# Optimization experiments

Measured on AMD Instinct MI355X. Metric: run time of the kernel, lower is better.

Reference implementation:

```python
import jax, jax.numpy as jnp
import numpy as np


def setup_inputs() -> dict:
    key = jax.random.key(0)
    k1, k2, k3, k4 = jax.random.split(key, 4)
    B, H, S, D = 2, 16, 2048, 64
    q = jax.random.normal(k1, (B, H, S, D), dtype=jnp.float32)
    k = jax.random.normal(k2, (B, H, S, D), dtype=jnp.float32)
    v = jax.random.normal(k3, (B, H, S, D), dtype=jnp.float32)
    mask = jax.random.randint(k4, (1, 1, S, S), 0, 2, dtype=jnp.int32)
    return {"q": q, "k": k, "v": v, "mask": mask}


def reference(q, k, v, mask):
    # scores: [B,H,S,S] -- intentionally materialized as in the original
    d = k.shape[-1]
    scale = 1.0 / jnp.sqrt(jnp.asarray(d, dtype=q.dtype))
    x = jnp.einsum("bhqd,bhkd->bhqk", q, k) * scale
    x = x + mask.astype(x.dtype) * jnp.asarray(-10000.0, dtype=x.dtype)
    p = jax.nn.softmax(x, axis=-1)  # dropout is identity in eval mode
    return jnp.einsum("bhqk,bhkd->bhqd", p, v)
```

## Files before the change

kernel.cpp:

```cpp
#include <hip/hip_runtime.h>


#define S_LEN 2048
#define D_DIM 64
#define N_KT 32
#define NBH 32
#define TILE_SEGS 20
#define TILE_SHORTS_P (TILE_SEGS * 512)
#define K_SHORTS 4608
#define SEG_U32 256

typedef __attribute__((ext_vector_type(8))) short bf16x8;
typedef __attribute__((ext_vector_type(16))) float f32x16;
typedef __attribute__((ext_vector_type(2))) __fp16 fp16x2;
typedef unsigned int u32;

#define C1 0.180336880111121f
#define CM (-14426.9504088896f)

static __device__ __forceinline__ unsigned short f2bf(float f) {
  union { float f; unsigned u; } x; x.f = f;
  return (unsigned short)((x.u + 0x8000u) >> 16);
}
static __device__ __forceinline__ unsigned packbf(float lo, float hi) {
  union { float f; unsigned u; } a, b; a.f = lo; b.f = hi;
  return ((a.u + 0x8000u) >> 16) | ((b.u + 0x8000u) & 0xffff0000u);
}
static __device__ __forceinline__ f32x16 zero16() {
  f32x16 z;
#pragma unroll
  for (int i = 0; i < 16; ++i) z[i] = 0.f;
  return z;
}
static __device__ __forceinline__ void dma16(const u32* g, u32* l) {
  __builtin_amdgcn_global_load_lds(
      (const __attribute__((address_space(1))) u32*)g,
      (__attribute__((address_space(3))) u32*)l, 16, 0, 0);
}
static __device__ __forceinline__ unsigned pkh(float lo, float hi) {
  union { fp16x2 h; unsigned u; } x;
  x.h = __builtin_amdgcn_cvt_pkrtz(lo, hi);
  return x.u;
}

__global__ __launch_bounds__(256) void prep_kv(
    const float* __restrict__ k, const float* __restrict__ v,
    unsigned short* __restrict__ kvws) {
  const int kt = blockIdx.x, bh = blockIdx.y;
  const int t = threadIdx.x;
  __shared__ unsigned short Vt[K_SHORTS];
  const size_t goff = (size_t)bh * (S_LEN * D_DIM) + (size_t)kt * 64 * D_DIM;
  const float4* kg = (const float4*)(k + goff);
  const float4* vg = (const float4*)(v + goff);
  unsigned short* kimg = kvws + (size_t)(bh * N_KT + kt) * TILE_SHORTS_P;
#pragma unroll
  for (int j = 0; j < 4; ++j) {
    const int i = t + j * 256;
    const int row = i >> 4, c4 = i & 15;
    const float4 x = kg[i];
    ushort4 w;
    w.x = f2bf(x.x); w.y = f2bf(x.y); w.z = f2bf(x.z); w.w = f2bf(x.w);
    *(ushort4*)&kimg[row * 72 + c4 * 4] = w;
    const float4 y = vg[i];
    const int swc = 8 * (((row >> 3) + c4) & 7) + (row & 7);
    const unsigned p01 = pkh(y.x, y.y);
    const unsigned p23 = pkh(y.z, y.w);
    Vt[(4 * c4 + 0) * 72 + swc] = (unsigned short)(p01 & 0xffff);
    Vt[(4 * c4 + 1) * 72 + swc] = (unsigned short)(p01 >> 16);
    Vt[(4 * c4 + 2) * 72 + swc] = (unsigned short)(p23 & 0xffff);
    Vt[(4 * c4 + 3) * 72 + swc] = (unsigned short)(p23 >> 16);
  }
  __syncthreads();
  uint4* vimg = (uint4*)(kimg + K_SHORTS);
  const uint4* lv = (const uint4*)Vt;
  for (int i = t; i < K_SHORTS / 8; i += 256) vimg[i] = lv[i];
}

__global__ __launch_bounds__(256) void prep_mask(
    const int* __restrict__ mask, u32* __restrict__ mw) {
  const int gt = blockIdx.x * 256 + threadIdx.x;
  const int q4 = gt & 3;
  const int kt = (gt >> 2) & 31;
  const int hl = (gt >> 7) & 1;
  const int row = gt >> 8;
  const int j0 = kt * 64 + 32 * (q4 >> 1) + 16 * (q4 & 1) + 4 * hl;
  const int* mr = mask + (size_t)row * S_LEN;
  const int4 a = *(const int4*)(mr + j0);
  const int4 b = *(const int4*)(mr + j0 + 8);
  uint4 w;
  w.x = (a.x == 0 ? 0x0000FFFFu : 0u) | (a.y == 0 ? 0xFFFF0000u : 0u);
  w.y = (a.z == 0 ? 0x0000FFFFu : 0u) | (a.w == 0 ? 0xFFFF0000u : 0u);
  w.z = (b.x == 0 ? 0x0000FFFFu : 0u) | (b.y == 0 ? 0xFFFF0000u : 0u);
  w.w = (b.z == 0 ? 0x0000FFFFu : 0u) | (b.w == 0 ? 0xFFFF0000u : 0u);
  *(uint4*)&mw[((size_t)(row * 2 + hl) * N_KT + kt) * 16 + q4 * 4] = w;
}

__global__ __launch_bounds__(256, 4) void attn_fwd(
    const float* __restrict__ q, const unsigned short* __restrict__ kvws,
    const u32* __restrict__ mw, float* __restrict__ out) {
  const int qt = blockIdx.x;
  const int bh = blockIdx.y;
  const size_t hoff = (size_t)bh * (S_LEN * D_DIM);

  __shared__ unsigned short sbuf[2][TILE_SHORTS_P];

  const int t = threadIdx.x;
  const int wave = t >> 6;
  const int lane = t & 63;
  const int col = lane & 31;
  const int hl = lane >> 5;
  const int sw = col >> 2;
  const int qh = wave >> 1;
  const int kh = wave & 1;
  const int qg = qt * 64 + qh * 32 + col;

  bf16x8 bQ[4];
  {
    const float* qrow = q + hoff + (size_t)qg * D_DIM;
#pragma unroll
    for (int ks = 0; ks < 4; ++ks) {
      const float4 x0 = *(const float4*)(qrow + ks * 16 + hl * 8);
      const float4 x1 = *(const float4*)(qrow + ks * 16 + hl * 8 + 4);
      union { bf16x8 v; unsigned d[4]; } u;
      u.d[0] = packbf(x0.x * C1, x0.y * C1);
      u.d[1] = packbf(x0.z * C1, x0.w * C1);
      u.d[2] = packbf(x1.x * C1, x1.y * C1);
      u.d[3] = packbf(x1.z * C1, x1.w * C1);
      bQ[ks] = u.v;
    }
  }

  f32x16 oT0 = zero16(), oT1 = zero16();
  float lacc0 = 0.f, lacc1 = 0.f;
  const uint4* mrow = (const uint4*)(mw + (size_t)(qg * 2 + hl) * N_KT * 16);
  const u32* img = (const u32*)(kvws + (size_t)bh * N_KT * TILE_SHORTS_P);
  const int seg0 = wave * 5;

#if __has_builtin(__builtin_amdgcn_fdot2)
  const fp16x2 ones2 = {(__fp16)1.0f, (__fp16)1.0f};
#endif

  uint4 mq0, mq1;
  {
    const uint4* mp = mrow + kh * 2;
    asm volatile("global_load_dwordx4 %0, %2, off\n\t"
                 "global_load_dwordx4 %1, %3, off"
                 : "=&v"(mq0), "=&v"(mq1)
                 : "v"(mp), "v"(mp + 1)
                 : "memory");
  }
#pragma unroll
  for (int s = 0; s < 5; ++s)
    dma16(img + (size_t)(seg0 + s) * SEG_U32 + lane * 4,
          (u32*)&sbuf[0][0] + (seg0 + s) * SEG_U32);
#pragma unroll
  for (int s = 0; s < 5; ++s)
    dma16(img + (size_t)(TILE_SEGS + seg0 + s) * SEG_U32 + lane * 4,
          (u32*)&sbuf[1][0] + (seg0 + s) * SEG_U32);

  for (int kt = 0; kt < N_KT; ++kt) {
    const int p = kt & 1;
    if (kt < N_KT - 1) {
      asm volatile("s_waitcnt vmcnt(5)" ::: "memory");
    } else {
      asm volatile("s_waitcnt vmcnt(0)" ::: "memory");
    }
    __builtin_amdgcn_s_barrier();
    __builtin_amdgcn_sched_barrier(0);

    const unsigned short* Ksb = &sbuf[p][0];
    const unsigned short* Vtb = &sbuf[p][K_SHORTS];
    const u32 mwv[8] = {mq0.x, mq0.y, mq0.z, mq0.w,
                        mq1.x, mq1.y, mq1.z, mq1.w};

    f32x16 sT = zero16();
#pragma unroll
    for (int ks = 0; ks < 4; ++ks) {
      const bf16x8 aK =
          *(const bf16x8*)&Ksb[(kh * 32 + col) * 72 + ks * 16 + hl * 8];
      sT = __builtin_amdgcn_mfma_f32_32x32x16_bf16(aK, bQ[ks], sT, 0, 0, 0);
    }

    unsigned pw[8];
#pragma unroll
    for (int g2 = 0; g2 < 4; ++g2) {
      const float e0 = __builtin_amdgcn_exp2f(sT[g2 * 4 + 0]);
      const float e1 = __builtin_amdgcn_exp2f(sT[g2 * 4 + 1]);
      const float e2 = __builtin_amdgcn_exp2f(sT[g2 * 4 + 2]);
      const float e3 = __builtin_amdgcn_exp2f(sT[g2 * 4 + 3]);
#if __has_builtin(__builtin_amdgcn_fdot2)
      const unsigned w0 = pkh(e0, e1) & mwv[g2 * 2 + 0];
      const unsigned w1 = pkh(e2, e3) & mwv[g2 * 2 + 1];
      pw[g2 * 2 + 0] = w0;
      pw[g2 * 2 + 1] = w1;
      union { unsigned u; fp16x2 h; } c0, c1;
      c0.u = w0; c1.u = w1;
      lacc0 = __builtin_amdgcn_fdot2(c0.h, ones2, lacc0, false);
      lacc1 = __builtin_amdgcn_fdot2(c1.h, ones2, lacc1, false);
#else
      const u32 mlo = mwv[g2 * 2 + 0], mhi = mwv[g2 * 2 + 1];
      const float e0m = (mlo & 0xFFFFu) ? e0 : 0.f;
      const float e1m = (mlo >> 16) ? e1 : 0.f;
      const float e2m = (mhi & 0xFFFFu) ? e2 : 0.f;
      const float e3m = (mhi >> 16) ? e3 : 0.f;
      pw[g2 * 2 + 0] = pkh(e0m, e1m);
      pw[g2 * 2 + 1] = pkh(e2m, e3m);
      lacc0 += e0m + e1m;
      lacc1 += e2m + e3m;
#endif
    }

#pragma unroll
    for (int ks2 = 0; ks2 < 2; ++ks2) {
      const unsigned d0 = pw[4 * ks2 + 0], d1 = pw[4 * ks2 + 1];
      const unsigned d2 = pw[4 * ks2 + 2], d3 = pw[4 * ks2 + 3];
      const unsigned s0 = hl ? d0 : d2;
      const unsigned s1 = hl ? d1 : d3;
      const unsigned r0 = (unsigned)__shfl_xor((int)s0, 32);
      const unsigned r1 = (unsigned)__shfl_xor((int)s1, 32);
      union { bf16x8 v; unsigned d[4]; } pf;
      pf.d[0] = hl ? r0 : d0;
      pf.d[1] = hl ? r1 : d1;
      pf.d[2] = hl ? d2 : r0;
      pf.d[3] = hl ? d3 : r1;
      const int cpr = 8 * (((4 * kh + 2 * ks2 + hl) + sw) & 7);
      const bf16x8 aV0 = *(const bf16x8*)&Vtb[col * 72 + cpr];
      const bf16x8 aV1 = *(const bf16x8*)&Vtb[(32 + col) * 72 + cpr];
      oT0 = __builtin_amdgcn_mfma_f32_32x32x16_f16(aV0, pf.v, oT0, 0, 0, 0);
      oT1 = __builtin_amdgcn_mfma_f32_32x32x16_f16(aV1, pf.v, oT1, 0, 0, 0);
    }

    if (kt < N_KT - 1) {
      asm volatile("s_waitcnt lgkmcnt(0)" ::: "memory");
      __builtin_amdgcn_s_barrier();
      __builtin_amdgcn_sched_barrier(0);
      {
        const uint4* mp = mrow + (kt + 1) * 4 + kh * 2;
        asm volatile("global_load_dwordx4 %0, %2, off\n\t"
                     "global_load_dwordx4 %1, %3, off"
                     : "=&v"(mq0), "=&v"(mq1)
                     : "v"(mp), "v"(mp + 1)
                     : "memory");
      }
      if (kt < N_KT - 2) {
        const u32* g = img + (size_t)(kt + 2) * (TILE_SEGS * SEG_U32);
#pragma unroll
        for (int s = 0; s < 5; ++s)
          dma16(g + (size_t)(seg0 + s) * SEG_U32 + lane * 4,
                (u32*)&sbuf[p][0] + (seg0 + s) * SEG_U32);
      }
    }
  }

  __syncthreads();
  {
    float* xb = (float*)&sbuf[0][0];
    float* lb = (float*)((char*)&sbuf[0][0] + 17408);
    const float lsum = lacc0 + lacc1;
    const float l2 = lsum + __shfl_xor(lsum, 32);
    float* xr = xb + (size_t)(qh * 32 + col) * 68;
    if (kh) {
#pragma unroll
      for (int rg = 0; rg < 4; ++rg) {
        float4 w0, w1;
        w0.x = oT0[rg * 4 + 0]; w0.y = oT0[rg * 4 + 1];
        w0.z = oT0[rg * 4 + 2]; w0.w = oT0[rg * 4 + 3];
        w1.x = oT1[rg * 4 + 0]; w1.y = oT1[rg * 4 + 1];
        w1.z = oT1[rg * 4 + 2]; w1.w = oT1[rg * 4 + 3];
        *(float4*)(xr + 8 * rg + 4 * hl) = w0;
        *(float4*)(xr + 32 + 8 * rg + 4 * hl) = w1;
      }
      if (!hl) lb[qh * 32 + col] = l2;
    }
    __syncthreads();
    if (!kh) {
      const float inv = 1.0f / (l2 + lb[qh * 32 + col]);
      float* orow = out + hoff + (size_t)qg * D_DIM;
#pragma unroll
      for (int rg = 0; rg < 4; ++rg) {
        const float4 a0 = *(const float4*)(xr + 8 * rg + 4 * hl);
        const float4 a1 = *(const float4*)(xr + 32 + 8 * rg + 4 * hl);
        float4 w0, w1;
        w0.x = (oT0[rg * 4 + 0] + a0.x) * inv;
        w0.y = (oT0[rg * 4 + 1] + a0.y) * inv;
        w0.z = (oT0[rg * 4 + 2] + a0.z) * inv;
        w0.w = (oT0[rg * 4 + 3] + a0.w) * inv;
        w1.x = (oT1[rg * 4 + 0] + a1.x) * inv;
        w1.y = (oT1[rg * 4 + 1] + a1.y) * inv;
        w1.z = (oT1[rg * 4 + 2] + a1.z) * inv;
        w1.w = (oT1[rg * 4 + 3] + a1.w) * inv;
        *(float4*)(orow + 8 * rg + 4 * hl) = w0;
        *(float4*)(orow + 32 + 8 * rg + 4 * hl) = w1;
      }
    }
  }
}

#define LDK 72
#define LDV 72
__global__ __launch_bounds__(256, 2) void attn_fwd_self(
    const float* __restrict__ q, const float* __restrict__ k,
    const float* __restrict__ v, const int* __restrict__ mask,
    float* __restrict__ out) {
  const int qt = blockIdx.x;
  const int bh = blockIdx.y;
  const size_t hoff = (size_t)bh * (S_LEN * D_DIM);
  __shared__ unsigned short Ks[64 * LDK];
  __shared__ unsigned short Vt[64 * LDV];
  const int t = threadIdx.x;
  const int wave = t >> 6;
  const int lane = t & 63;
  const int col = lane & 31;
  const int hl = lane >> 5;
  const int sw = col >> 2;
  const int qg = qt * 128 + wave * 32 + col;
  bf16x8 bQ[4];
  {
    const float* qrow = q + hoff + (size_t)qg * D_DIM;
#pragma unroll
    for (int ks = 0; ks < 4; ++ks) {
      const float4 x0 = *(const float4*)(qrow + ks * 16 + hl * 8);
      const float4 x1 = *(const float4*)(qrow + ks * 16 + hl * 8 + 4);
      union { bf16x8 v; unsigned d[4]; } u;
      u.d[0] = packbf(x0.x, x0.y);
      u.d[1] = packbf(x0.z, x0.w);
      u.d[2] = packbf(x1.x, x1.y);
      u.d[3] = packbf(x1.z, x1.w);
      bQ[ks] = u.v;
    }
  }
  float4 pk[4], pv[4];
  {
    const float4* kg = (const float4*)(k + hoff);
    const float4* vg = (const float4*)(v + hoff);
#pragma unroll
    for (int j = 0; j < 4; ++j) { pk[j] = kg[t + j * 256]; pv[j] = vg[t + j * 256]; }
  }
  f32x16 oT0 = zero16(), oT1 = zero16();
  float lacc = 0.f;
  const int* mrow = mask + (size_t)qg * S_LEN;
  for (int kt = 0; kt < N_KT; ++kt) {
    __syncthreads();
#pragma unroll
    for (int j = 0; j < 4; ++j) {
      const int i = t + j * 256;
      const int row = i >> 4, c4 = i & 15;
      ushort4 w;
      w.x = f2bf(pk[j].x); w.y = f2bf(pk[j].y);
      w.z = f2bf(pk[j].z); w.w = f2bf(pk[j].w);
      *(ushort4*)&Ks[row * LDK + c4 * 4] = w;
      const int swc = 8 * (((row >> 3) + c4) & 7) + (row & 7);
      Vt[(4 * c4 + 0) * LDV + swc] = f2bf(pv[j].x);
      Vt[(4 * c4 + 1) * LDV + swc] = f2bf(pv[j].y);
      Vt[(4 * c4 + 2) * LDV + swc] = f2bf(pv[j].z);
      Vt[(4 * c4 + 3) * LDV + swc] = f2bf(pv[j].w);
    }
    __syncthreads();
    if (kt + 1 < N_KT) {
      const float4* kg = (const float4*)(k + hoff + (size_t)(kt + 1) * 64 * D_DIM);
      const float4* vg = (const float4*)(v + hoff + (size_t)(kt + 1) * 64 * D_DIM);
#pragma unroll
      for (int j = 0; j < 4; ++j) { pk[j] = kg[t + j * 256]; pv[j] = vg[t + j * 256]; }
    }
    int4 mq[2][4];
#pragma unroll
    for (int kb = 0; kb < 2; ++kb)
#pragma unroll
      for (int g = 0; g < 4; ++g)
        mq[kb][g] = *(const int4*)(mrow + kt * 64 + kb * 32 + g * 8 + hl * 4);
    f32x16 sT0 = zero16(), sT1 = zero16();
#pragma unroll
    for (int ks = 0; ks < 4; ++ks) {
      const bf16x8 aK0 = *(const bf16x8*)&Ks[col * LDK + ks * 16 + hl * 8];
      const bf16x8 aK1 = *(const bf16x8*)&Ks[(32 + col) * LDK + ks * 16 + hl * 8];
      sT0 = __builtin_amdgcn_mfma_f32_32x32x16_bf16(aK0, bQ[ks], sT0, 0, 0, 0);
      sT1 = __builtin_amdgcn_mfma_f32_32x32x16_bf16(aK1, bQ[ks], sT1, 0, 0, 0);
    }
    unsigned pw[2][8];
#pragma unroll
    for (int kb = 0; kb < 2; ++kb) {
      const f32x16 sT = kb ? sT1 : sT0;
      float e[16];
#pragma unroll
      for (int g = 0; g < 4; ++g) {
        const int4 mv = mq[kb][g];
        const int* mvp = &mv.x;
#pragma unroll
        for (int r3 = 0; r3 < 4; ++r3) {
          const int reg = g * 4 + r3;
          const float bias = mvp[r3] ? CM : 0.0f;
          const float ev = __builtin_amdgcn_exp2f(fmaf(sT[reg], C1, bias));
          e[reg] = ev;
          lacc += ev;
        }
        pw[kb][g * 2 + 0] = packbf(e[g * 4 + 0], e[g * 4 + 1]);
        pw[kb][g * 2 + 1] = packbf(e[g * 4 + 2], e[g * 4 + 3]);
      }
    }
#pragma unroll
    for (int ks = 0; ks < 4; ++ks) {
      const int kb = ks >> 1, h = ks & 1;
      const unsigned d0 = pw[kb][4 * h + 0], d1 = pw[kb][4 * h + 1];
      const unsigned d2 = pw[kb][4 * h + 2], d3 = pw[kb][4 * h + 3];
      const unsigned s0 = hl ? d0 : d2;
      const unsigned s1 = hl ? d1 : d3;
      const unsigned r0 = (unsigned)__shfl_xor((int)s0, 32);
      const unsigned r1 = (unsigned)__shfl_xor((int)s1, 32);
      union { bf16x8 v; unsigned d[4]; } pf;
      pf.d[0] = hl ? r0 : d0;
      pf.d[1] = hl ? r1 : d1;
      pf.d[2] = hl ? d2 : r0;
      pf.d[3] = hl ? d3 : r1;
      const int cpr = 8 * (((2 * ks + hl) + sw) & 7);
      const bf16x8 aV0 = *(const bf16x8*)&Vt[col * LDV + cpr];
      const bf16x8 aV1 = *(const bf16x8*)&Vt[(32 + col) * LDV + cpr];
      oT0 = __builtin_amdgcn_mfma_f32_32x32x16_bf16(aV0, pf.v, oT0, 0, 0, 0);
      oT1 = __builtin_amdgcn_mfma_f32_32x32x16_bf16(aV1, pf.v, oT1, 0, 0, 0);
    }
  }
  const float ltot = lacc + __shfl_xor(lacc, 32);
  const float inv = 1.0f / ltot;
  float* orow = out + hoff + (size_t)qg * D_DIM;
#pragma unroll
  for (int rg = 0; rg < 4; ++rg) {
    float4 w0, w1;
    w0.x = oT0[rg * 4 + 0] * inv; w0.y = oT0[rg * 4 + 1] * inv;
    w0.z = oT0[rg * 4 + 2] * inv; w0.w = oT0[rg * 4 + 3] * inv;
    w1.x = oT1[rg * 4 + 0] * inv; w1.y = oT1[rg * 4 + 1] * inv;
    w1.z = oT1[rg * 4 + 2] * inv; w1.w = oT1[rg * 4 + 3] * inv;
    *(float4*)(orow + 8 * rg + 4 * hl) = w0;
    *(float4*)(orow + 32 + 8 * rg + 4 * hl) = w1;
  }
}

extern "C" void kernel_launch(void* const* d_in, const int* in_sizes, int n_in,
                              void* d_out, int out_size, void* d_ws, size_t ws_size,
                              hipStream_t stream) {
  const float* q = (const float*)d_in[0];
  const float* k = (const float*)d_in[1];
  const float* v = (const float*)d_in[2];
  const int* mask = (const int*)d_in[3];
  float* out = (float*)d_out;

  const size_t kv_shorts = (size_t)NBH * N_KT * TILE_SHORTS_P;
  const size_t mw_words = (size_t)S_LEN * 2 * N_KT * 16;
  const size_t need = kv_shorts * sizeof(unsigned short) + mw_words * 4;

  if (ws_size >= need) {
    unsigned short* kvws = (unsigned short*)d_ws;
    u32* mwp = (u32*)(kvws + kv_shorts);
    prep_kv<<<dim3(N_KT, NBH), dim3(256), 0, stream>>>(k, v, kvws);
    prep_mask<<<dim3((S_LEN * 2 * N_KT * 4) / 256), dim3(256), 0, stream>>>(mask, mwp);
    attn_fwd<<<dim3(S_LEN / 64, NBH), dim3(256), 0, stream>>>(q, kvws, mwp, out);
  } else {
    attn_fwd_self<<<dim3(S_LEN / 128, NBH), dim3(256), 0, stream>>>(q, k, v, mask, out);
  }
}
```

Baseline: 167.3 us.

## Fuse KV and mask prep kernels and store K/V tiles in MFMA fragment order

The two preprocessing kernels are merged into one launch, with the block index deciding whether a block converts K/V or packs the mask. The K/V workspace image changes from padded 72-stride rows with swizzled V to a dense fragment-ordered layout, so each lane's MFMA operand is a contiguous 16-byte chunk. Tiles shrink from 20 to 16 segments, which cuts DMA traffic and LDS footprint per tile and removes the swizzle arithmetic in the main loop. The cost is more shuffling work in the prep kernel, including a scalar gather when transposing V.

```diff
diff --git a/kernel.cpp b/kernel.cpp
--- a/kernel.cpp
+++ b/kernel.cpp
@@ -5,9 +5,8 @@
 #define D_DIM 64
 #define N_KT 32
 #define NBH 32
-#define TILE_SEGS 20
-#define TILE_SHORTS_P (TILE_SEGS * 512)
-#define K_SHORTS 4608
+#define TILE_SEGS 16
+#define TILE_SHORTS 8192
 #define SEG_U32 256
 
 typedef __attribute__((ext_vector_type(8))) short bf16x8;
@@ -43,56 +42,63 @@
   return x.u;
 }
 
-__global__ __launch_bounds__(256) void prep_kv(
+__global__ __launch_bounds__(256) void prep_fused(
     const float* __restrict__ k, const float* __restrict__ v,
-    unsigned short* __restrict__ kvws) {
-  const int kt = blockIdx.x, bh = blockIdx.y;
+    const int* __restrict__ mask, unsigned short* __restrict__ kvws,
+    u32* __restrict__ mw) {
+  __shared__ unsigned short Kr[64 * 72];
+  __shared__ unsigned short Vr[64 * 72];
+  const int blk = blockIdx.x;
   const int t = threadIdx.x;
-  __shared__ unsigned short Vt[K_SHORTS];
-  const size_t goff = (size_t)bh * (S_LEN * D_DIM) + (size_t)kt * 64 * D_DIM;
-  const float4* kg = (const float4*)(k + goff);
-  const float4* vg = (const float4*)(v + goff);
-  unsigned short* kimg = kvws + (size_t)(bh * N_KT + kt) * TILE_SHORTS_P;
-#pragma unroll
-  for (int j = 0; j < 4; ++j) {
-    const int i = t + j * 256;
-    const int row = i >> 4, c4 = i & 15;
-    const float4 x = kg[i];
-    ushort4 w;
-    w.x = f2bf(x.x); w.y = f2bf(x.y); w.z = f2bf(x.z); w.w = f2bf(x.w);
-    *(ushort4*)&kimg[row * 72 + c4 * 4] = w;
-    const float4 y = vg[i];
-    const int swc = 8 * (((row >> 3) + c4) & 7) + (row & 7);
-    const unsigned p01 = pkh(y.x, y.y);
-    const unsigned p23 = pkh(y.z, y.w);
-    Vt[(4 * c4 + 0) * 72 + swc] = (unsigned short)(p01 & 0xffff);
-    Vt[(4 * c4 + 1) * 72 + swc] = (unsigned short)(p01 >> 16);
-    Vt[(4 * c4 + 2) * 72 + swc] = (unsigned short)(p23 & 0xffff);
-    Vt[(4 * c4 + 3) * 72 + swc] = (unsigned short)(p23 >> 16);
-  }
-  __syncthreads();
-  uint4* vimg = (uint4*)(kimg + K_SHORTS);
-  const uint4* lv = (const uint4*)Vt;
-  for (int i = t; i < K_SHORTS / 8; i += 256) vimg[i] = lv[i];
-}
-
-__global__ __launch_bounds__(256) void prep_mask(
-    const int* __restrict__ mask, u32* __restrict__ mw) {
-  const int gt = blockIdx.x * 256 + threadIdx.x;
-  const int q4 = gt & 3;
-  const int kt = (gt >> 2) & 31;
-  const int hl = (gt >> 7) & 1;
-  const int row = gt >> 8;
-  const int j0 = kt * 64 + 32 * (q4 >> 1) + 16 * (q4 & 1) + 4 * hl;
-  const int* mr = mask + (size_t)row * S_LEN;
-  const int4 a = *(const int4*)(mr + j0);
-  const int4 b = *(const int4*)(mr + j0 + 8);
-  uint4 w;
-  w.x = (a.x == 0 ? 0x0000FFFFu : 0u) | (a.y == 0 ? 0xFFFF0000u : 0u);
-  w.y = (a.z == 0 ? 0x0000FFFFu : 0u) | (a.w == 0 ? 0xFFFF0000u : 0u);
-  w.z = (b.x == 0 ? 0x0000FFFFu : 0u) | (b.y == 0 ? 0xFFFF0000u : 0u);
-  w.w = (b.z == 0 ? 0x0000FFFFu : 0u) | (b.w == 0 ? 0xFFFF0000u : 0u);
-  *(uint4*)&mw[((size_t)(row * 2 + hl) * N_KT + kt) * 16 + q4 * 4] = w;
+  if (blk < N_KT * NBH) {
+    const int kt = blk & 31, bh = blk >> 5;
+    const size_t goff = (size_t)bh * (S_LEN * D_DIM) + (size_t)kt * 64 * D_DIM;
+    const float4* kg = (const float4*)(k + goff);
+    const float4* vg = (const float4*)(v + goff);
+#pragma unroll
+    for (int j = 0; j < 4; ++j) {
+      const int i = t + j * 256;
+      const int row = i >> 4, c4 = i & 15;
+      const float4 x = kg[i];
+      ushort4 w;
+      w.x = f2bf(x.x); w.y = f2bf(x.y); w.z = f2bf(x.z); w.w = f2bf(x.w);
+      *(ushort4*)&Kr[row * 72 + c4 * 4] = w;
+      const float4 y = vg[i];
+      const unsigned p01 = pkh(y.x, y.y), p23 = pkh(y.z, y.w);
+      uint2 vv; vv.x = p01; vv.y = p23;
+      *(uint2*)&Vr[row * 72 + c4 * 4] = vv;
+    }
+    __syncthreads();
+    uint4* img = (uint4*)(kvws + (size_t)(bh * N_KT + kt) * TILE_SHORTS);
+    for (int c = t; c < 512; c += 256) {
+      const int col = c & 31, hlc = (c >> 5) & 1, ks = (c >> 6) & 3, khc = c >> 8;
+      img[c] = *(const uint4*)&Kr[(khc * 32 + col) * 72 + ks * 16 + hlc * 8];
+    }
+    for (int c = t; c < 512; c += 256) {
+      const int col = c & 31, b = (c >> 5) & 1, hlc = (c >> 6) & 1, kcHi = c >> 7;
+      const int d = b * 32 + col, kk = (2 * kcHi + hlc) * 8;
+      union { unsigned short s[8]; uint4 u; } o;
+#pragma unroll
+      for (int jj = 0; jj < 8; ++jj) o.s[jj] = Vr[(kk + jj) * 72 + d];
+      img[512 + c] = o.u;
+    }
+  } else {
+    const int gt = (blk - N_KT * NBH) * 256 + t;
+    const int q4 = gt & 3;
+    const int kt = (gt >> 2) & 31;
+    const int hl = (gt >> 7) & 1;
+    const int row = gt >> 8;
+    const int j0 = kt * 64 + 32 * (q4 >> 1) + 16 * (q4 & 1) + 4 * hl;
+    const int* mr = mask + (size_t)row * S_LEN;
+    const int4 a = *(const int4*)(mr + j0);
+    const int4 b = *(const int4*)(mr + j0 + 8);
+    uint4 w;
+    w.x = (a.x == 0 ? 0x0000FFFFu : 0u) | (a.y == 0 ? 0xFFFF0000u : 0u);
+    w.y = (a.z == 0 ? 0x0000FFFFu : 0u) | (a.w == 0 ? 0xFFFF0000u : 0u);
+    w.z = (b.x == 0 ? 0x0000FFFFu : 0u) | (b.y == 0 ? 0xFFFF0000u : 0u);
+    w.w = (b.z == 0 ? 0x0000FFFFu : 0u) | (b.w == 0 ? 0xFFFF0000u : 0u);
+    *(uint4*)&mw[((size_t)(row * 2 + hl) * N_KT + kt) * 16 + q4 * 4] = w;
+  }
 }
 
 __global__ __launch_bounds__(256, 4) void attn_fwd(
@@ -102,14 +108,13 @@
   const int bh = blockIdx.y;
   const size_t hoff = (size_t)bh * (S_LEN * D_DIM);
 
-  __shared__ unsigned short sbuf[2][TILE_SHORTS_P];
+  __shared__ unsigned short sbuf[2][TILE_SHORTS];
 
   const int t = threadIdx.x;
   const int wave = t >> 6;
   const int lane = t & 63;
   const int col = lane & 31;
   const int hl = lane >> 5;
-  const int sw = col >> 2;
   const int qh = wave >> 1;
   const int kh = wave & 1;
   const int qg = qt * 64 + qh * 32 + col;
@@ -133,8 +138,8 @@
   f32x16 oT0 = zero16(), oT1 = zero16();
   float lacc0 = 0.f, lacc1 = 0.f;
   const uint4* mrow = (const uint4*)(mw + (size_t)(qg * 2 + hl) * N_KT * 16);
-  const u32* img = (const u32*)(kvws + (size_t)bh * N_KT * TILE_SHORTS_P);
-  const int seg0 = wave * 5;
+  const u32* img = (const u32*)(kvws + (size_t)bh * N_KT * TILE_SHORTS);
+  const int seg0 = wave * 4;
 
 #if __has_builtin(__builtin_amdgcn_fdot2)
   const fp16x2 ones2 = {(__fp16)1.0f, (__fp16)1.0f};
@@ -150,18 +155,18 @@
                  : "memory");
   }
 #pragma unroll
-  for (int s = 0; s < 5; ++s)
+  for (int s = 0; s < 4; ++s)
     dma16(img + (size_t)(seg0 + s) * SEG_U32 + lane * 4,
           (u32*)&sbuf[0][0] + (seg0 + s) * SEG_U32);
 #pragma unroll
-  for (int s = 0; s < 5; ++s)
+  for (int s = 0; s < 4; ++s)
     dma16(img + (size_t)(TILE_SEGS + seg0 + s) * SEG_U32 + lane * 4,
           (u32*)&sbuf[1][0] + (seg0 + s) * SEG_U32);
 
   for (int kt = 0; kt < N_KT; ++kt) {
     const int p = kt & 1;
     if (kt < N_KT - 1) {
-      asm volatile("s_waitcnt vmcnt(5)" ::: "memory");
+      asm volatile("s_waitcnt vmcnt(4)" ::: "memory");
     } else {
       asm volatile("s_waitcnt vmcnt(0)" ::: "memory");
     }
@@ -169,7 +174,7 @@
     __builtin_amdgcn_sched_barrier(0);
 
     const unsigned short* Ksb = &sbuf[p][0];
-    const unsigned short* Vtb = &sbuf[p][K_SHORTS];
+    const unsigned short* Vtb = &sbuf[p][4096];
     const u32 mwv[8] = {mq0.x, mq0.y, mq0.z, mq0.w,
                         mq1.x, mq1.y, mq1.z, mq1.w};
 
@@ -177,7 +182,7 @@
 #pragma unroll
     for (int ks = 0; ks < 4; ++ks) {
       const bf16x8 aK =
-          *(const bf16x8*)&Ksb[(kh * 32 + col) * 72 + ks * 16 + hl * 8];
+          *(const bf16x8*)&Ksb[kh * 2048 + ks * 512 + hl * 256 + col * 8];
       sT = __builtin_amdgcn_mfma_f32_32x32x16_bf16(aK, bQ[ks], sT, 0, 0, 0);
     }
 
@@ -223,9 +228,11 @@
       pf.d[1] = hl ? r1 : d1;
       pf.d[2] = hl ? d2 : r0;
       pf.d[3] = hl ? d3 : r1;
-      const int cpr = 8 * (((4 * kh + 2 * ks2 + hl) + sw) & 7);
-      const bf16x8 aV0 = *(const bf16x8*)&Vtb[col * 72 + cpr];
-      const bf16x8 aV1 = *(const bf16x8*)&Vtb[(32 + col) * 72 + cpr];
+      const int kcHi = kh * 2 + ks2;
+      const bf16x8 aV0 =
+          *(const bf16x8*)&Vtb[kcHi * 1024 + hl * 512 + 0 * 256 + col * 8];
+      const bf16x8 aV1 =
+          *(const bf16x8*)&Vtb[kcHi * 1024 + hl * 512 + 1 * 256 + col * 8];
       oT0 = __builtin_amdgcn_mfma_f32_32x32x16_f16(aV0, pf.v, oT0, 0, 0, 0);
       oT1 = __builtin_amdgcn_mfma_f32_32x32x16_f16(aV1, pf.v, oT1, 0, 0, 0);
     }
@@ -245,7 +252,7 @@
       if (kt < N_KT - 2) {
         const u32* g = img + (size_t)(kt + 2) * (TILE_SEGS * SEG_U32);
 #pragma unroll
-        for (int s = 0; s < 5; ++s)
+        for (int s = 0; s < 4; ++s)
           dma16(g + (size_t)(seg0 + s) * SEG_U32 + lane * 4,
                 (u32*)&sbuf[p][0] + (seg0 + s) * SEG_U32);
       }
@@ -442,15 +449,15 @@
   const int* mask = (const int*)d_in[3];
   float* out = (float*)d_out;
 
-  const size_t kv_shorts = (size_t)NBH * N_KT * TILE_SHORTS_P;
+  const size_t kv_shorts = (size_t)NBH * N_KT * TILE_SHORTS;
   const size_t mw_words = (size_t)S_LEN * 2 * N_KT * 16;
   const size_t need = kv_shorts * sizeof(unsigned short) + mw_words * 4;
 
   if (ws_size >= need) {
     unsigned short* kvws = (unsigned short*)d_ws;
     u32* mwp = (u32*)(kvws + kv_shorts);
-    prep_kv<<<dim3(N_KT, NBH), dim3(256), 0, stream>>>(k, v, kvws);
-    prep_mask<<<dim3((S_LEN * 2 * N_KT * 4) / 256), dim3(256), 0, stream>>>(mask, mwp);
+    prep_fused<<<dim3(N_KT * NBH + (S_LEN * 2 * N_KT * 4) / 256), dim3(256), 0,
+                 stream>>>(k, v, mask, kvws, mwp);
     attn_fwd<<<dim3(S_LEN / 64, NBH), dim3(256), 0, stream>>>(q, kvws, mwp, out);
   } else {
     attn_fwd_self<<<dim3(S_LEN / 128, NBH), dim3(256), 0, stream>>>(q, k, v, mask, out);
```

Result: faster. 163.9 us (-2.0%).
